# Kernel tuning notes

Hardware: AMD Instinct MI355X
Metric: run time of the kernel (lower is better)

Reference implementation:

```python
import jax, jax.numpy as jnp
import numpy as np

D = 256; H = 8; L = 4; P = 4; DFF = 1024
B = 4; NQ = 900
SHAPES = np.array([[100, 160], [50, 80], [25, 40], [13, 20]], dtype=np.int64)
NV = int((SHAPES[:, 0] * SHAPES[:, 1]).sum())


def setup_inputs():
    key = jax.random.key(0)
    ks = jax.random.split(key, 16)
    def w(k, shape):
        return jax.random.normal(k, shape, jnp.float32) * 0.02
    return {
        "tgt": jax.random.normal(ks[0], (B, NQ, D), jnp.float32),
        "tgt_query_pos": jax.random.normal(ks[1], (B, NQ, D), jnp.float32),
        "tgt_reference_points": jax.random.uniform(ks[2], (B, NQ, L, 2), dtype=jnp.float32),
        "memory": jax.random.normal(ks[3], (B, NV, D), jnp.float32),
        "value_proj_w": w(ks[4], (D, D)), "value_proj_b": jnp.zeros((D,), jnp.float32),
        "samp_off_w": w(ks[5], (H * L * P * 2, D)), "samp_off_b": jnp.zeros((H * L * P * 2,), jnp.float32),
        "attn_w_w": w(ks[6], (H * L * P, D)), "attn_w_b": jnp.zeros((H * L * P,), jnp.float32),
        "ca_out_w": w(ks[7], (D, D)), "ca_out_b": jnp.zeros((D,), jnp.float32),
        "ln1_g": jnp.ones((D,), jnp.float32), "ln1_b": jnp.zeros((D,), jnp.float32),
        "in_proj_w": w(ks[8], (3 * D, D)), "in_proj_b": jnp.zeros((3 * D,), jnp.float32),
        "sa_out_w": w(ks[9], (D, D)), "sa_out_b": jnp.zeros((D,), jnp.float32),
        "ln2_g": jnp.ones((D,), jnp.float32), "ln2_b": jnp.zeros((D,), jnp.float32),
        "ffn1_w": w(ks[10], (DFF, D)), "ffn1_b": jnp.zeros((DFF,), jnp.float32),
        "ffn2_w": w(ks[11], (D, DFF)), "ffn2_b": jnp.zeros((D,), jnp.float32),
        "ln3_g": jnp.ones((D,), jnp.float32), "ln3_b": jnp.zeros((D,), jnp.float32),
        "spatial_shapes": jnp.asarray(SHAPES),
    }


def layer_norm(x, g, b, eps=1e-5):
    m = x.mean(-1, keepdims=True)
    v = ((x - m) ** 2).mean(-1, keepdims=True)
    return (x - m) / jnp.sqrt(v + eps) * g + b


def ms_deform_attn(query, refp, value, shapes, Wv, bv, Wo, bo, Wa, ba, Wout, bout):
    # query [B,Nq,D], refp [B,Nq,L,2] in [0,1], value [B,NV,D]; shapes: np [L,2] (H,W)
    Bq, Nq, Dm = query.shape
    dh = Dm // H
    v = (value @ Wv.T + bv).reshape(Bq, -1, H, dh)
    off = (query @ Wo.T + bo).reshape(Bq, Nq, H, L, P, 2)
    aw = jax.nn.softmax((query @ Wa.T + ba).reshape(Bq, Nq, H, L * P), axis=-1)
    aw = aw.reshape(Bq, Nq, H, L, P)
    norm = jnp.asarray(np.stack([shapes[:, 1], shapes[:, 0]], -1), jnp.float32)  # [L,2] = (W,H)
    loc = refp[:, :, None, :, None, :] + off / norm[None, None, None, :, None, :]  # [B,Nq,H,L,P,2]
    starts = np.concatenate([[0], np.cumsum(shapes[:, 0] * shapes[:, 1])])
    acc = jnp.zeros((Bq, Nq, H, dh), query.dtype)
    for l in range(L):
        Hl, Wl = int(shapes[l, 0]), int(shapes[l, 1])
        vf = v[:, int(starts[l]):int(starts[l]) + Hl * Wl]                 # [B,HW,H,dh]
        v2 = vf.transpose(0, 2, 1, 3).reshape(Bq * H, Hl * Wl, dh)
        # grid_sample align_corners=False: pixel = loc*size - 0.5
        xl = loc[:, :, :, l, :, 0] * Wl - 0.5                              # [B,Nq,H,P]
        yl = loc[:, :, :, l, :, 1] * Hl - 0.5
        x0 = jnp.floor(xl); y0 = jnp.floor(yl)
        wx = xl - x0; wy = yl - y0
        x0i = x0.astype(jnp.int32); y0i = y0.astype(jnp.int32)
        def corner(xi, yi, wgt):
            valid = (xi >= 0) & (xi < Wl) & (yi >= 0) & (yi < Hl)
            idx = jnp.clip(yi, 0, Hl - 1) * Wl + jnp.clip(xi, 0, Wl - 1)   # [B,Nq,H,P]
            idx2 = idx.transpose(0, 2, 1, 3).reshape(Bq * H, Nq * P)
            g = jnp.take_along_axis(v2, idx2[..., None], axis=1)           # [B*H,Nq*P,dh]
            g = g.reshape(Bq, H, Nq, P, dh).transpose(0, 2, 1, 3, 4)
            return g * (wgt * valid).astype(query.dtype)[..., None]
        s = (corner(x0i, y0i, (1 - wx) * (1 - wy))
             + corner(x0i + 1, y0i, wx * (1 - wy))
             + corner(x0i, y0i + 1, (1 - wx) * wy)
             + corner(x0i + 1, y0i + 1, wx * wy))                          # [B,Nq,H,P,dh]
        acc = acc + jnp.einsum('bqhpd,bqhp->bqhd', s, aw[:, :, :, l])
    return acc.reshape(Bq, Nq, Dm) @ Wout.T + bout


def mha(q, k, v, Win, bin_, Wout, bout):
    Dm = q.shape[-1]; dh = Dm // H
    def proj(x, W, b):
        return (x @ W.T + b).reshape(x.shape[0], x.shape[1], H, dh)
    qh = proj(q, Win[:Dm], bin_[:Dm])
    kh = proj(k, Win[Dm:2 * Dm], bin_[Dm:2 * Dm])
    vh = proj(v, Win[2 * Dm:], bin_[2 * Dm:])
    att = jax.nn.softmax(jnp.einsum('bqhd,bkhd->bhqk', qh, kh) / np.sqrt(dh).astype(np.float32), axis=-1)
    o = jnp.einsum('bhqk,bkhd->bqhd', att, vh).reshape(q.shape[0], q.shape[1], Dm)
    return o @ Wout.T + bout


def _forward(tgt, tgt_query_pos, tgt_reference_points, memory,
             value_proj_w, value_proj_b, samp_off_w, samp_off_b, attn_w_w, attn_w_b,
             ca_out_w, ca_out_b, ln1_g, ln1_b, in_proj_w, in_proj_b, sa_out_w, sa_out_b,
             ln2_g, ln2_b, ffn1_w, ffn1_b, ffn2_w, ffn2_b, ln3_g, ln3_b, shapes):
    # cross (deformable) attention
    q = tgt + tgt_query_pos
    tgt2 = ms_deform_attn(q, tgt_reference_points, memory, shapes,
                          value_proj_w, value_proj_b, samp_off_w, samp_off_b,
                          attn_w_w, attn_w_b, ca_out_w, ca_out_b)
    x = layer_norm(tgt + tgt2, ln1_g, ln1_b)
    # self attention (q=k=x+pos, v=x)
    qk = x + tgt_query_pos
    x = layer_norm(x + mha(qk, qk, x, in_proj_w, in_proj_b, sa_out_w, sa_out_b), ln2_g, ln2_b)
    # FFN
    ff = jax.nn.relu(x @ ffn1_w.T + ffn1_b) @ ffn2_w.T + ffn2_b
    return layer_norm(x + ff, ln3_g, ln3_b)


def reference(tgt, tgt_query_pos, tgt_reference_points, memory,
              value_proj_w, value_proj_b, samp_off_w, samp_off_b, attn_w_w, attn_w_b,
              ca_out_w, ca_out_b, ln1_g, ln1_b, in_proj_w, in_proj_b, sa_out_w, sa_out_b,
              ln2_g, ln2_b, ffn1_w, ffn1_b, ffn2_w, ffn2_b, ln3_g, ln3_b, spatial_shapes):
    shapes = np.asarray(spatial_shapes)
    return _forward(tgt, tgt_query_pos, tgt_reference_points, memory,
                    value_proj_w, value_proj_b, samp_off_w, samp_off_b, attn_w_w, attn_w_b,
                    ca_out_w, ca_out_b, ln1_g, ln1_b, in_proj_w, in_proj_b, sa_out_w, sa_out_b,
                    ln2_g, ln2_b, ffn1_w, ffn1_b, ffn2_w, ffn2_b, ln3_g, ln3_b, shapes)
```

## Files before the change

kernel.cpp:

```cpp
#include <hip/hip_runtime.h>

constexpr int D_   = 256;
constexpr int H_   = 8;
constexpr int DH   = 32;
constexpr int L_   = 4;
constexpr int P_   = 4;
constexpr int DFF_ = 1024;
constexpr int B_   = 4;
constexpr int NQ_  = 900;
constexpr int NV_  = 21260;
constexpr int MQ   = B_ * NQ_;
constexpr int MV   = B_ * NV_;

typedef __attribute__((ext_vector_type(8))) short short8;
typedef __attribute__((ext_vector_type(4))) float f32x4;

static __device__ __forceinline__ unsigned short f2bf(float x) {
  union { float f; unsigned int u; } v;
  v.f = x;
  const unsigned int r = v.u + 0x7fffu + ((v.u >> 16) & 1u);
  return (unsigned short)(r >> 16);
}
static __device__ __forceinline__ float bf2f(unsigned short u) {
  union { unsigned int i; float f; } x;
  x.i = ((unsigned int)u) << 16;
  return x.f;
}

struct CvtArgs {
  const float* src[9];
  unsigned short* dst[9];
  int n[9];
  float scl[9];
};

__global__ __launch_bounds__(256) void cvtw(CvtArgs a) {
  const int seg = blockIdx.y;
  const int n = a.n[seg];
  const float s = a.scl[seg];
  const float* __restrict__ sp = a.src[seg];
  unsigned short* __restrict__ d = a.dst[seg];
  for (int i = (blockIdx.x * 256 + threadIdx.x) * 4; i < n;
       i += gridDim.x * 256 * 4) {
    const float4 v = *reinterpret_cast<const float4*>(&sp[i]);
    d[i + 0] = f2bf(v.x * s); d[i + 1] = f2bf(v.y * s);
    d[i + 2] = f2bf(v.z * s); d[i + 3] = f2bf(v.w * s);
  }
}

__global__ void biasprep(const float* __restrict__ bin,
                         const float* __restrict__ bo,
                         const float* __restrict__ ba,
                         float* __restrict__ bqkv, float* __restrict__ bfu) {
  const int i = threadIdx.x;
  if (i < 768) bqkv[i] = (i < 256) ? bin[i] * 0.17677669529663687f : bin[i];
  if (i < 384) bfu[i] = (i < 256) ? bo[i] : ba[i - 256];
}

template <bool ABF, bool ADD2, bool RELU, bool OUTBF>
__global__ __launch_bounds__(256) void gemm_db(
    const void* __restrict__ Ap, const float* __restrict__ A2,
    const unsigned short* __restrict__ Wbf, const float* __restrict__ bias,
    void* __restrict__ Cp, int M, int N, int K) {
  constexpr int LDR = 40;
  __shared__ unsigned short As[2][128][LDR];
  __shared__ unsigned short Bs[2][128][LDR];

  const float* Af = (const float*)Ap;
  const unsigned short* Ab = (const unsigned short*)Ap;
  float* Cf = (float*)Cp;
  unsigned short* Cb = (unsigned short*)Cp;

  const int t    = threadIdx.x;
  const int wave = t >> 6;
  const int l    = t & 63;
  const int n0   = blockIdx.x * 128;
  const int m0   = blockIdx.y * 128;
  const int wm   = (wave >> 1) * 64;
  const int wn   = (wave & 1) * 64;
  const int srow = t >> 1;
  const int sseg = (t & 1) * 16;
  const int lr   = l & 15;
  const int lk   = (l >> 4) * 8;

  const int am = m0 + srow;
  const bool aok = am < M;
  const size_t arow = (size_t)am * K;
  const size_t brow = (size_t)(n0 + srow) * K;

  f32x4 acc[4][4];
#pragma unroll
  for (int i = 0; i < 4; ++i)
#pragma unroll
    for (int j = 0; j < 4; ++j) acc[i][j] = (f32x4)0.f;

  short8 ar0, ar1, br0, br1;

  auto LOAD = [&](int k0) {
    if constexpr (ABF) {
      if (aok) {
        ar0 = *reinterpret_cast<const short8*>(&Ab[arow + k0 + sseg]);
        ar1 = *reinterpret_cast<const short8*>(&Ab[arow + k0 + sseg + 8]);
      } else {
        ar0 = (short8)(short)0; ar1 = (short8)(short)0;
      }
    } else {
      if (aok) {
        float f[16];
#pragma unroll
        for (int j = 0; j < 4; ++j) {
          const float4 av =
              *reinterpret_cast<const float4*>(&Af[arow + k0 + sseg + 4 * j]);
          f[4 * j + 0] = av.x; f[4 * j + 1] = av.y;
          f[4 * j + 2] = av.z; f[4 * j + 3] = av.w;
        }
        if constexpr (ADD2) {
#pragma unroll
          for (int j = 0; j < 4; ++j) {
            const float4 av =
                *reinterpret_cast<const float4*>(&A2[arow + k0 + sseg + 4 * j]);
            f[4 * j + 0] += av.x; f[4 * j + 1] += av.y;
            f[4 * j + 2] += av.z; f[4 * j + 3] += av.w;
          }
        }
        alignas(16) unsigned short u[16];
#pragma unroll
        for (int j = 0; j < 16; ++j) u[j] = f2bf(f[j]);
        ar0 = *reinterpret_cast<short8*>(&u[0]);
        ar1 = *reinterpret_cast<short8*>(&u[8]);
      } else {
        ar0 = (short8)(short)0; ar1 = (short8)(short)0;
      }
    }
    br0 = *reinterpret_cast<const short8*>(&Wbf[brow + k0 + sseg]);
    br1 = *reinterpret_cast<const short8*>(&Wbf[brow + k0 + sseg + 8]);
  };

  const int nt = K >> 5;
  LOAD(0);
  for (int tt = 0; tt < nt; ++tt) {
    const int cur = tt & 1;
    *reinterpret_cast<short8*>(&As[cur][srow][sseg])     = ar0;
    *reinterpret_cast<short8*>(&As[cur][srow][sseg + 8]) = ar1;
    *reinterpret_cast<short8*>(&Bs[cur][srow][sseg])     = br0;
    *reinterpret_cast<short8*>(&Bs[cur][srow][sseg + 8]) = br1;
    if (tt + 1 < nt) LOAD((tt + 1) << 5);
    __syncthreads();

    short8 af[4], bfr[4];
#pragma unroll
    for (int fi = 0; fi < 4; ++fi)
      af[fi] = *reinterpret_cast<const short8*>(&As[cur][wm + fi * 16 + lr][lk]);
#pragma unroll
    for (int fj = 0; fj < 4; ++fj)
      bfr[fj] = *reinterpret_cast<const short8*>(&Bs[cur][wn + fj * 16 + lr][lk]);

#pragma unroll
    for (int fi = 0; fi < 4; ++fi)
#pragma unroll
      for (int fj = 0; fj < 4; ++fj)
        acc[fi][fj] = __builtin_amdgcn_mfma_f32_16x16x32_bf16(
            af[fi], bfr[fj], acc[fi][fj], 0, 0, 0);
  }

  const int orow = (l >> 4) * 4;
#pragma unroll
  for (int fi = 0; fi < 4; ++fi) {
#pragma unroll
    for (int fj = 0; fj < 4; ++fj) {
      const int n = n0 + wn + fj * 16 + lr;
      const float bn = bias[n];
#pragma unroll
      for (int i = 0; i < 4; ++i) {
        const int m = m0 + wm + fi * 16 + orow + i;
        if (m < M) {
          float vv = acc[fi][fj][i] + bn;
          if (RELU) vv = fmaxf(vv, 0.f);
          if (OUTBF)
            Cb[(size_t)m * N + n] = f2bf(vv);
          else
            Cf[(size_t)m * N + n] = vv;
        }
      }
    }
  }
}

template <int K, bool ABF, bool ADD2, bool RELU, bool OUTBF>
__global__ __launch_bounds__(256) void gemm_p2(
    const void* __restrict__ Ap, const float* __restrict__ A2,
    const unsigned short* __restrict__ Wbf, const float* __restrict__ bias,
    void* __restrict__ Cp, int M, int N) {
  constexpr int LDR = 40;
  constexpr int NT = K / 32;
  __shared__ unsigned short As[2][128][LDR];
  __shared__ unsigned short Bs[2][128][LDR];

  const float* Af = (const float*)Ap;
  const unsigned short* Ab = (const unsigned short*)Ap;
  float* Cf = (float*)Cp;
  unsigned short* Cb = (unsigned short*)Cp;

  const int t    = threadIdx.x;
  const int wave = t >> 6;
  const int l    = t & 63;
  const int n0   = blockIdx.x * 128;
  const int m0   = blockIdx.y * 128;
  const int wm   = (wave >> 1) * 64;
  const int wn   = (wave & 1) * 64;
  const int srow = t >> 1;
  const int sseg = (t & 1) * 16;
  const int lr   = l & 15;
  const int lk   = (l >> 4) * 8;

  const int am = m0 + srow;
  const bool aok = am < M;
  const size_t arow = (size_t)am * K;
  const size_t brow = (size_t)(n0 + srow) * K;

  f32x4 acc[4][4];
#pragma unroll
  for (int i = 0; i < 4; ++i)
#pragma unroll
    for (int j = 0; j < 4; ++j) acc[i][j] = (f32x4)0.f;

  float  frA[16], frB[16];
  short8 abA0, abA1, abB0, abB1;
  short8 brA0, brA1, brB0, brB1;

#define LOAD_SLOT(SUF, k0)                                                     \
  do {                                                                         \
    if constexpr (ABF) {                                                       \
      if (aok) {                                                               \
        ab##SUF##0 = *reinterpret_cast<const short8*>(&Ab[arow + (k0) + sseg]);\
        ab##SUF##1 = *reinterpret_cast<const short8*>(&Ab[arow + (k0) + sseg + 8]);\
      } else {                                                                 \
        ab##SUF##0 = (short8)(short)0; ab##SUF##1 = (short8)(short)0;          \
      }                                                                        \
    } else {                                                                   \
      if (aok) {                                                               \
        _Pragma("unroll")                                                      \
        for (int j = 0; j < 4; ++j) {                                          \
          const float4 av =                                                    \
              *reinterpret_cast<const float4*>(&Af[arow + (k0) + sseg + 4 * j]);\
          fr##SUF[4 * j + 0] = av.x; fr##SUF[4 * j + 1] = av.y;                \
          fr##SUF[4 * j + 2] = av.z; fr##SUF[4 * j + 3] = av.w;                \
        }                                                                      \
        if constexpr (ADD2) {                                                  \
          _Pragma("unroll")                                                    \
          for (int j = 0; j < 4; ++j) {                                        \
            const float4 av =                                                  \
                *reinterpret_cast<const float4*>(&A2[arow + (k0) + sseg + 4 * j]);\
            fr##SUF[4 * j + 0] += av.x; fr##SUF[4 * j + 1] += av.y;            \
            fr##SUF[4 * j + 2] += av.z; fr##SUF[4 * j + 3] += av.w;            \
          }                                                                    \
        }                                                                      \
      } else {                                                                 \
        _Pragma("unroll")                                                      \
        for (int j = 0; j < 16; ++j) fr##SUF[j] = 0.f;                         \
      }                                                                        \
    }                                                                          \
    br##SUF##0 = *reinterpret_cast<const short8*>(&Wbf[brow + (k0) + sseg]);   \
    br##SUF##1 = *reinterpret_cast<const short8*>(&Wbf[brow + (k0) + sseg + 8]);\
  } while (0)

#define WRITE_SLOT(SUF, BUF)                                                   \
  do {                                                                         \
    if constexpr (ABF) {                                                       \
      *reinterpret_cast<short8*>(&As[BUF][srow][sseg])     = ab##SUF##0;       \
      *reinterpret_cast<short8*>(&As[BUF][srow][sseg + 8]) = ab##SUF##1;       \
    } else {                                                                   \
      alignas(16) unsigned short u[16];                                        \
      _Pragma("unroll")                                                        \
      for (int j = 0; j < 16; ++j) u[j] = f2bf(fr##SUF[j]);                    \
      *reinterpret_cast<short8*>(&As[BUF][srow][sseg]) =                       \
          *reinterpret_cast<short8*>(&u[0]);                                   \
      *reinterpret_cast<short8*>(&As[BUF][srow][sseg + 8]) =                   \
          *reinterpret_cast<short8*>(&u[8]);                                   \
    }                                                                          \
    *reinterpret_cast<short8*>(&Bs[BUF][srow][sseg])     = br##SUF##0;         \
    *reinterpret_cast<short8*>(&Bs[BUF][srow][sseg + 8]) = br##SUF##1;         \
  } while (0)

#define MFMA_STEP(BUF)                                                         \
  do {                                                                         \
    short8 af0 = *reinterpret_cast<const short8*>(&As[BUF][wm +  0 + lr][lk]); \
    short8 af1 = *reinterpret_cast<const short8*>(&As[BUF][wm + 16 + lr][lk]); \
    short8 af2 = *reinterpret_cast<const short8*>(&As[BUF][wm + 32 + lr][lk]); \
    short8 af3 = *reinterpret_cast<const short8*>(&As[BUF][wm + 48 + lr][lk]); \
    short8 bf0 = *reinterpret_cast<const short8*>(&Bs[BUF][wn +  0 + lr][lk]); \
    short8 bf1 = *reinterpret_cast<const short8*>(&Bs[BUF][wn + 16 + lr][lk]); \
    short8 bf2 = *reinterpret_cast<const short8*>(&Bs[BUF][wn + 32 + lr][lk]); \
    short8 bf3 = *reinterpret_cast<const short8*>(&Bs[BUF][wn + 48 + lr][lk]); \
    acc[0][0] = __builtin_amdgcn_mfma_f32_16x16x32_bf16(af0, bf0, acc[0][0], 0, 0, 0); \
    acc[0][1] = __builtin_amdgcn_mfma_f32_16x16x32_bf16(af0, bf1, acc[0][1], 0, 0, 0); \
    acc[0][2] = __builtin_amdgcn_mfma_f32_16x16x32_bf16(af0, bf2, acc[0][2], 0, 0, 0); \
    acc[0][3] = __builtin_amdgcn_mfma_f32_16x16x32_bf16(af0, bf3, acc[0][3], 0, 0, 0); \
    acc[1][0] = __builtin_amdgcn_mfma_f32_16x16x32_bf16(af1, bf0, acc[1][0], 0, 0, 0); \
    acc[1][1] = __builtin_amdgcn_mfma_f32_16x16x32_bf16(af1, bf1, acc[1][1], 0, 0, 0); \
    acc[1][2] = __builtin_amdgcn_mfma_f32_16x16x32_bf16(af1, bf2, acc[1][2], 0, 0, 0); \
    acc[1][3] = __builtin_amdgcn_mfma_f32_16x16x32_bf16(af1, bf3, acc[1][3], 0, 0, 0); \
    acc[2][0] = __builtin_amdgcn_mfma_f32_16x16x32_bf16(af2, bf0, acc[2][0], 0, 0, 0); \
    acc[2][1] = __builtin_amdgcn_mfma_f32_16x16x32_bf16(af2, bf1, acc[2][1], 0, 0, 0); \
    acc[2][2] = __builtin_amdgcn_mfma_f32_16x16x32_bf16(af2, bf2, acc[2][2], 0, 0, 0); \
    acc[2][3] = __builtin_amdgcn_mfma_f32_16x16x32_bf16(af2, bf3, acc[2][3], 0, 0, 0); \
    acc[3][0] = __builtin_amdgcn_mfma_f32_16x16x32_bf16(af3, bf0, acc[3][0], 0, 0, 0); \
    acc[3][1] = __builtin_amdgcn_mfma_f32_16x16x32_bf16(af3, bf1, acc[3][1], 0, 0, 0); \
    acc[3][2] = __builtin_amdgcn_mfma_f32_16x16x32_bf16(af3, bf2, acc[3][2], 0, 0, 0); \
    acc[3][3] = __builtin_amdgcn_mfma_f32_16x16x32_bf16(af3, bf3, acc[3][3], 0, 0, 0); \
  } while (0)

  LOAD_SLOT(A, 0);
  LOAD_SLOT(B, 32);
#pragma unroll
  for (int tt = 0; tt < NT; tt += 2) {
    WRITE_SLOT(A, 0);
    if (tt + 2 < NT) LOAD_SLOT(A, (tt + 2) * 32);
    __syncthreads();
    MFMA_STEP(0);

    WRITE_SLOT(B, 1);
    if (tt + 3 < NT) LOAD_SLOT(B, (tt + 3) * 32);
    __syncthreads();
    MFMA_STEP(1);
  }
#undef LOAD_SLOT
#undef WRITE_SLOT
#undef MFMA_STEP

  const int orow = (l >> 4) * 4;
#pragma unroll
  for (int fi = 0; fi < 4; ++fi) {
#pragma unroll
    for (int fj = 0; fj < 4; ++fj) {
      const int n = n0 + wn + fj * 16 + lr;
      const float bn = bias[n];
#pragma unroll
      for (int i = 0; i < 4; ++i) {
        const int m = m0 + wm + fi * 16 + orow + i;
        if (m < M) {
          float vv = acc[fi][fj][i] + bn;
          if (RELU) vv = fmaxf(vv, 0.f);
          if (OUTBF)
            Cb[(size_t)m * N + n] = f2bf(vv);
          else
            Cf[(size_t)m * N + n] = vv;
        }
      }
    }
  }
}

template <bool ABF, bool ADD2, bool RELU, bool OUTBF>
__global__ __launch_bounds__(256) void gemm_bres(
    const void* __restrict__ Ap, const float* __restrict__ A2,
    const unsigned short* __restrict__ Wbf, const float* __restrict__ bias,
    void* __restrict__ Cp, int M, int N, int add_nlim) {
  __shared__ unsigned short Bs[32768];
  __shared__ unsigned short As[2][64][40];

  const float* Af = (const float*)Ap;
  const unsigned short* Ab = (const unsigned short*)Ap;
  float* Cf = (float*)Cp;
  unsigned short* Cb = (unsigned short*)Cp;

  const int t    = threadIdx.x;
  const int wave = t >> 6;
  const int l    = t & 63;
  const int n0   = blockIdx.x * 128;
  const int m0   = blockIdx.y * 64;
  const int wm   = (wave >> 1) * 32;
  const int wcg  = (wave & 1) * 4;
  const int lr   = l & 15;
  const int lk8  = (l >> 4) * 8;
  const bool doadd = ADD2 && (n0 < add_nlim);

#pragma unroll
  for (int i = 0; i < 16; ++i) {
    const int e  = i * 256 + t;
    const int el = e & 63;
    const int cg = (e >> 6) & 7;
    const int st = e >> 9;
    const int row = n0 + cg * 16 + (el & 15);
    const int col = st * 32 + ((el >> 4) * 8);
    *reinterpret_cast<short8*>(&Bs[e * 8]) =
        *reinterpret_cast<const short8*>(&Wbf[(size_t)row * 256 + col]);
  }

  const int arow = t >> 2;
  const int acol = (t & 3) * 8;
  const int am   = m0 + arow;
  const bool aok = am < M;
  const size_t abase = (size_t)am * 256 + acol;

  float  fr[3][8];
  short8 br_[3];

  auto ALOAD = [&](int slot, int tt) {
    const int k0 = tt * 32;
    if constexpr (ABF) {
      br_[slot] = aok ? *reinterpret_cast<const short8*>(&Ab[abase + k0])
                      : (short8)(short)0;
    } else {
      if (aok) {
        const float4 a0 = *reinterpret_cast<const float4*>(&Af[abase + k0]);
        const float4 a1 = *reinterpret_cast<const float4*>(&Af[abase + k0 + 4]);
        fr[slot][0] = a0.x; fr[slot][1] = a0.y;
        fr[slot][2] = a0.z; fr[slot][3] = a0.w;
        fr[slot][4] = a1.x; fr[slot][5] = a1.y;
        fr[slot][6] = a1.z; fr[slot][7] = a1.w;
        if constexpr (ADD2) {
          if (doadd) {
            const float4 b0 = *reinterpret_cast<const float4*>(&A2[abase + k0]);
            const float4 b1 = *reinterpret_cast<const float4*>(&A2[abase + k0 + 4]);
            fr[slot][0] += b0.x; fr[slot][1] += b0.y;
            fr[slot][2] += b0.z; fr[slot][3] += b0.w;
            fr[slot][4] += b1.x; fr[slot][5] += b1.y;
            fr[slot][6] += b1.z; fr[slot][7] += b1.w;
          }
        }
      } else {
#pragma unroll
        for (int j = 0; j < 8; ++j) fr[slot][j] = 0.f;
      }
    }
  };
  auto AWRITE = [&](int slot, int tt) {
    if constexpr (ABF) {
      *reinterpret_cast<short8*>(&As[tt & 1][arow][acol]) = br_[slot];
    } else {
      alignas(16) unsigned short u[8];
#pragma unroll
      for (int j = 0; j < 8; ++j) u[j] = f2bf(fr[slot][j]);
      *reinterpret_cast<short8*>(&As[tt & 1][arow][acol]) =
          *reinterpret_cast<short8*>(&u[0]);
    }
  };

  f32x4 acc[2][4];
#pragma unroll
  for (int fi = 0; fi < 2; ++fi)
#pragma unroll
    for (int fj = 0; fj < 4; ++fj) acc[fi][fj] = (f32x4)0.f;

  ALOAD(0, 0); ALOAD(1, 1); ALOAD(2, 2);

#pragma unroll
  for (int tt = 0; tt < 8; ++tt) {
    AWRITE(tt % 3, tt);
    if (tt + 3 < 8) ALOAD(tt % 3, tt + 3);
    __syncthreads();

    short8 afr[2];
#pragma unroll
    for (int fi = 0; fi < 2; ++fi)
      afr[fi] = *reinterpret_cast<const short8*>(&As[tt & 1][wm + fi * 16 + lr][lk8]);

#pragma unroll
    for (int fj = 0; fj < 4; ++fj) {
      const short8 bfr = *reinterpret_cast<const short8*>(
          &Bs[(((tt * 8) + wcg + fj) * 64 + l) * 8]);
      acc[0][fj] = __builtin_amdgcn_mfma_f32_16x16x32_bf16(afr[0], bfr, acc[0][fj], 0, 0, 0);
      acc[1][fj] = __builtin_amdgcn_mfma_f32_16x16x32_bf16(afr[1], bfr, acc[1][fj], 0, 0, 0);
    }
  }

  const int or4 = (l >> 4) * 4;
#pragma unroll
  for (int fi = 0; fi < 2; ++fi) {
#pragma unroll
    for (int fj = 0; fj < 4; ++fj) {
      const int n = n0 + (wave & 1) * 64 + fj * 16 + lr;
      const float bn = bias[n];
#pragma unroll
      for (int i = 0; i < 4; ++i) {
        const int m = m0 + wm + fi * 16 + or4 + i;
        if (m < M) {
          float vv = acc[fi][fj][i] + bn;
          if (RELU) vv = fmaxf(vv, 0.f);
          if (OUTBF)
            Cb[(size_t)m * N + n] = f2bf(vv);
          else
            Cf[(size_t)m * N + n] = vv;
        }
      }
    }
  }
}

__global__ __launch_bounds__(256) void deform(const float* __restrict__ refp,
                                              const float* __restrict__ offlog,
                                              const unsigned short* __restrict__ v,
                                              float* __restrict__ acc) {
  __shared__ float aw[2][128];
  const int t  = threadIdx.x;
  const int tq = t >> 7;
  const int tt = t & 127;
  const int bq = blockIdx.x * 2 + tq;
  const int b  = bq / NQ_;
  const int h  = tt >> 4;
  const int dd = tt & 15;

  aw[tq][tt] = offlog[(size_t)bq * 384 + 256 + tt];
  __syncthreads();
  if (t < 16) {
    const int q = t >> 3, hh = t & 7;
    float* a = &aw[q][hh * 16];
    float mx = -1e30f;
#pragma unroll
    for (int i = 0; i < 16; ++i) mx = fmaxf(mx, a[i]);
    float e[16], s = 0.f;
#pragma unroll
    for (int i = 0; i < 16; ++i) { e[i] = expf(a[i] - mx); s += e[i]; }
    const float inv = 1.f / s;
#pragma unroll
    for (int i = 0; i < 16; ++i) a[i] = e[i] * inv;
  }
  __syncthreads();

  constexpr int ST[4] = {0, 16000, 20000, 21000};
  constexpr int HL[4] = {100, 50, 25, 13};
  constexpr int WL[4] = {160, 80, 40, 20};

  float a0 = 0.f, a1 = 0.f;
#pragma unroll
  for (int l = 0; l < L_; ++l) {
    const float rx = refp[(bq * L_ + l) * 2 + 0];
    const float ry = refp[(bq * L_ + l) * 2 + 1];
    const float Wf = (float)WL[l], Hf = (float)HL[l];
    const int   Wi = WL[l], Hi = HL[l];
    const size_t vbase = (size_t)(b * NV_ + ST[l]) * D_ + h * DH + dd * 2;
#pragma unroll
    for (int p = 0; p < P_; ++p) {
      const float ox = offlog[(size_t)bq * 384 + h * 32 + l * 8 + p * 2 + 0];
      const float oy = offlog[(size_t)bq * 384 + h * 32 + l * 8 + p * 2 + 1];
      const float locx = rx + ox / Wf;
      const float locy = ry + oy / Hf;
      const float xl = locx * Wf - 0.5f;
      const float yl = locy * Hf - 0.5f;
      const float x0 = floorf(xl), y0 = floorf(yl);
      const float wx = xl - x0, wy = yl - y0;
      const int x0i = (int)x0, y0i = (int)y0;
      const float w = aw[tq][h * 16 + l * 4 + p];

      float s0 = 0.f, s1 = 0.f;
#pragma unroll
      for (int c = 0; c < 4; ++c) {
        const int xi = x0i + (c & 1);
        const int yi = y0i + (c >> 1);
        const float cw = ((c & 1) ? wx : 1.f - wx) * ((c >> 1) ? wy : 1.f - wy);
        const bool valid = (xi >= 0) && (xi < Wi) && (yi >= 0) && (yi < Hi);
        const int xc = min(max(xi, 0), Wi - 1);
        const int yc = min(max(yi, 0), Hi - 1);
        const unsigned int g2 = *reinterpret_cast<const unsigned int*>(
            &v[vbase + (size_t)(yc * Wi + xc) * D_]);
        const float g0 = bf2f((unsigned short)(g2 & 0xffffu));
        const float g1 = bf2f((unsigned short)(g2 >> 16));
        s0 += valid ? g0 * cw : 0.f;
        s1 += valid ? g1 * cw : 0.f;
      }
      a0 += w * s0;
      a1 += w * s1;
    }
  }
  acc[(size_t)bq * D_ + h * DH + dd * 2 + 0] = a0;
  acc[(size_t)bq * D_ + h * DH + dd * 2 + 1] = a1;
}

constexpr int TQM  = 64;
constexpr int NQTM = (NQ_ + TQM - 1) / TQM;

__global__ __launch_bounds__(256) void mha_mfma(
    const unsigned short* __restrict__ qkvh,
    unsigned short* __restrict__ o) {
  __shared__ unsigned short Qs[64][40];
  __shared__ unsigned short Ks[64][40];
  __shared__ unsigned short Vts[32][72];
  __shared__ unsigned short Ps[64][72];

  const int bx = blockIdx.x;
  const int qt = bx % NQTM;
  const int h  = (bx / NQTM) % H_;
  const int b  = bx / (NQTM * H_);
  const int t  = threadIdx.x;
  const int wave = t >> 6;
  const int l    = t & 63;
  const int q0   = qt * TQM;
  const int wrow = wave * 16;
  const int lr   = l & 15;
  const int lkb  = (l >> 4) * 8;

  {
    const int r = t >> 2, cb = (t & 3) * 8;
    short8 u;
    if (q0 + r < NQ_)
      u = *reinterpret_cast<const short8*>(
          &qkvh[(size_t)(b * NQ_ + q0 + r) * 768 + h * DH + cb]);
    else
      u = (short8)(short)0;
    *reinterpret_cast<short8*>(&Qs[r][cb]) = u;
  }
  __syncthreads();

  const short8 qa = *reinterpret_cast<const short8*>(&Qs[wrow + lr][lkb]);

  f32x4 oacc[2];
  oacc[0] = (f32x4)0.f; oacc[1] = (f32x4)0.f;
  float m_[4] = {-1e30f, -1e30f, -1e30f, -1e30f};
  float l_[4] = {0.f, 0.f, 0.f, 0.f};

  for (int kt = 0; kt < NQTM; ++kt) {
    const int k0 = kt * 64;
    const int nk = min(64, NQ_ - k0);
    __syncthreads();

    {
      const int r = t >> 2, cb = (t & 3) * 8;
      short8 u;
      if (r < nk)
        u = *reinterpret_cast<const short8*>(
            &qkvh[(size_t)(b * NQ_ + k0 + r) * 768 + 256 + h * DH + cb]);
      else
        u = (short8)(short)0;
      *reinterpret_cast<short8*>(&Ks[r][cb]) = u;
    }
    {
      const int k = t & 63, db = (t >> 6) * 8;
      short8 u;
      if (k < nk)
        u = *reinterpret_cast<const short8*>(
            &qkvh[(size_t)(b * NQ_ + k0 + k) * 768 + 512 + h * DH + db]);
      else
        u = (short8)(short)0;
#pragma unroll
      for (int j = 0; j < 8; ++j) Vts[db + j][k] = (unsigned short)u[j];
    }
    __syncthreads();

    f32x4 sacc[4];
#pragma unroll
    for (int fj = 0; fj < 4; ++fj)
      sacc[fj] = __builtin_amdgcn_mfma_f32_16x16x32_bf16(
          qa, *reinterpret_cast<const short8*>(&Ks[16 * fj + lr][lkb]),
          (f32x4)0.f, 0, 0, 0);

    bool cv[4];
#pragma unroll
    for (int fj = 0; fj < 4; ++fj) cv[fj] = (16 * fj + lr) < nk;

    float p0[4], p1[4], p2[4], p3[4], sc_[4];
#pragma unroll
    for (int i = 0; i < 4; ++i) {
      float tm = -1e30f;
      if (cv[0]) tm = fmaxf(tm, sacc[0][i]);
      if (cv[1]) tm = fmaxf(tm, sacc[1][i]);
      if (cv[2]) tm = fmaxf(tm, sacc[2][i]);
      if (cv[3]) tm = fmaxf(tm, sacc[3][i]);
      tm = fmaxf(tm, __shfl_xor(tm, 1));
      tm = fmaxf(tm, __shfl_xor(tm, 2));
      tm = fmaxf(tm, __shfl_xor(tm, 4));
      tm = fmaxf(tm, __shfl_xor(tm, 8));
      const float mn = fmaxf(m_[i], tm);
      sc_[i] = __expf(m_[i] - mn);
      m_[i] = mn;
      const float e0 = cv[0] ? __expf(sacc[0][i] - mn) : 0.f;
      const float e1 = cv[1] ? __expf(sacc[1][i] - mn) : 0.f;
      const float e2 = cv[2] ? __expf(sacc[2][i] - mn) : 0.f;
      const float e3 = cv[3] ? __expf(sacc[3][i] - mn) : 0.f;
      p0[i] = e0; p1[i] = e1; p2[i] = e2; p3[i] = e3;
      float rs = e0 + e1 + e2 + e3;
      rs += __shfl_xor(rs, 1);
      rs += __shfl_xor(rs, 2);
      rs += __shfl_xor(rs, 4);
      rs += __shfl_xor(rs, 8);
      l_[i] = l_[i] * sc_[i] + rs;
    }

#pragma unroll
    for (int i = 0; i < 4; ++i) {
      const int pr = wrow + (l >> 4) * 4 + i;
      Ps[pr][0  + lr] = f2bf(p0[i]);
      Ps[pr][16 + lr] = f2bf(p1[i]);
      Ps[pr][32 + lr] = f2bf(p2[i]);
      Ps[pr][48 + lr] = f2bf(p3[i]);
    }
    __syncthreads();

    const short8 pa0 = *reinterpret_cast<const short8*>(&Ps[wrow + lr][lkb]);
    const short8 pa1 = *reinterpret_cast<const short8*>(&Ps[wrow + lr][lkb + 32]);
#pragma unroll
    for (int nt = 0; nt < 2; ++nt) {
      f32x4 c = oacc[nt];
#pragma unroll
      for (int i = 0; i < 4; ++i) c[i] *= sc_[i];
      c = __builtin_amdgcn_mfma_f32_16x16x32_bf16(
          pa0, *reinterpret_cast<const short8*>(&Vts[16 * nt + lr][lkb]), c, 0, 0, 0);
      c = __builtin_amdgcn_mfma_f32_16x16x32_bf16(
          pa1, *reinterpret_cast<const short8*>(&Vts[16 * nt + lr][lkb + 32]), c, 0, 0, 0);
      oacc[nt] = c;
    }
  }

#pragma unroll
  for (int i = 0; i < 4; ++i) {
    const int r = (l >> 4) * 4 + i;
    const int q = q0 + wrow + r;
    if (q < NQ_) {
      const float inv = 1.f / l_[i];
      o[(size_t)(b * NQ_ + q) * D_ + h * DH + 0  + lr] = f2bf(oacc[0][i] * inv);
      o[(size_t)(b * NQ_ + q) * D_ + h * DH + 16 + lr] = f2bf(oacc[1][i] * inv);
    }
  }
}

__global__ __launch_bounds__(256) void ln(const float* __restrict__ res,
                                          const float* __restrict__ add,
                                          const float* __restrict__ g,
                                          const float* __restrict__ bt,
                                          float* __restrict__ out) {
  __shared__ float red[256];
  const int r = blockIdx.x, t = threadIdx.x;
  const float x = res[r * D_ + t] + add[r * D_ + t];
  red[t] = x;
  __syncthreads();
  for (int s = 128; s > 0; s >>= 1) {
    if (t < s) red[t] += red[t + s];
    __syncthreads();
  }
  const float mean = red[0] * (1.f / D_);
  __syncthreads();
  const float dx = x - mean;
  red[t] = dx * dx;
  __syncthreads();
  for (int s = 128; s > 0; s >>= 1) {
    if (t < s) red[t] += red[t + s];
    __syncthreads();
  }
  const float var = red[0] * (1.f / D_);
  out[r * D_ + t] = dx * rsqrtf(var + 1e-5f) * g[t] + bt[t];
}

extern "C" void kernel_launch(void* const* d_in, const int* in_sizes, int n_in,
                              void* d_out, int out_size, void* d_ws,
                              size_t ws_size, hipStream_t stream) {
  const float* tgt   = (const float*)d_in[0];
  const float* pos   = (const float*)d_in[1];
  const float* refp  = (const float*)d_in[2];
  const float* mem   = (const float*)d_in[3];
  const float* Wv    = (const float*)d_in[4];
  const float* bv    = (const float*)d_in[5];
  const float* Wo    = (const float*)d_in[6];
  const float* bo    = (const float*)d_in[7];
  const float* Wa    = (const float*)d_in[8];
  const float* ba    = (const float*)d_in[9];
  const float* Wca   = (const float*)d_in[10];
  const float* bca   = (const float*)d_in[11];
  const float* g1    = (const float*)d_in[12];
  const float* b1    = (const float*)d_in[13];
  const float* Win   = (const float*)d_in[14];
  const float* bin   = (const float*)d_in[15];
  const float* Wsa   = (const float*)d_in[16];
  const float* bsa   = (const float*)d_in[17];
  const float* g2    = (const float*)d_in[18];
  const float* b2    = (const float*)d_in[19];
  const float* W1    = (const float*)d_in[20];
  const float* bb1   = (const float*)d_in[21];
  const float* W2    = (const float*)d_in[22];
  const float* bb2   = (const float*)d_in[23];
  const float* g3    = (const float*)d_in[24];
  const float* b3    = (const float*)d_in[25];

  char* cur = (char*)d_ws;
  auto alloc = [&](size_t bytes) {
    char* p = cur;
    cur += (bytes + 255) & ~(size_t)255;
    return (void*)p;
  };
  unsigned short* v_bf    = (unsigned short*)alloc((size_t)MV * 256 * 2);
  float*          offlog  = (float*)alloc((size_t)MQ * 384 * 4);
  float*          accb    = (float*)alloc((size_t)MQ * 256 * 4);
  float*          tmp     = (float*)alloc((size_t)MQ * 256 * 4);
  float*          x1      = (float*)alloc((size_t)MQ * 256 * 4);
  float*          x2      = (float*)alloc((size_t)MQ * 256 * 4);
  unsigned short* qkvh_bf = (unsigned short*)alloc((size_t)MQ * 768 * 2);
  unsigned short* obuf_bf = (unsigned short*)alloc((size_t)MQ * 256 * 2);
  unsigned short* h1_bf   = (unsigned short*)alloc((size_t)MQ * 1024 * 2);
  unsigned short* Wv_bf   = (unsigned short*)alloc(65536 * 2);
  unsigned short* Wfu_bf  = (unsigned short*)alloc(98304 * 2);
  unsigned short* Wca_bf  = (unsigned short*)alloc(65536 * 2);
  unsigned short* Win_bf  = (unsigned short*)alloc(196608 * 2);
  unsigned short* Wsa_bf  = (unsigned short*)alloc(65536 * 2);
  unsigned short* W1_bf   = (unsigned short*)alloc(262144 * 2);
  unsigned short* W2_bf   = (unsigned short*)alloc(262144 * 2);
  float*          biasqkv = (float*)alloc(768 * 4);
  float*          bfused  = (float*)alloc(384 * 4);

  const float qscale = 0.17677669529663687f;

  CvtArgs ca;
  ca.src[0] = Wv;            ca.dst[0] = Wv_bf;          ca.n[0] = 65536;  ca.scl[0] = 1.f;
  ca.src[1] = Wo;            ca.dst[1] = Wfu_bf;         ca.n[1] = 65536;  ca.scl[1] = 1.f;
  ca.src[2] = Wa;            ca.dst[2] = Wfu_bf + 65536; ca.n[2] = 32768;  ca.scl[2] = 1.f;
  ca.src[3] = Wca;           ca.dst[3] = Wca_bf;         ca.n[3] = 65536;  ca.scl[3] = 1.f;
  ca.src[4] = Win;           ca.dst[4] = Win_bf;         ca.n[4] = 65536;  ca.scl[4] = qscale;
  ca.src[5] = Win + 65536;   ca.dst[5] = Win_bf + 65536; ca.n[5] = 131072; ca.scl[5] = 1.f;
  ca.src[6] = Wsa;           ca.dst[6] = Wsa_bf;         ca.n[6] = 65536;  ca.scl[6] = 1.f;
  ca.src[7] = W1;            ca.dst[7] = W1_bf;          ca.n[7] = 262144; ca.scl[7] = 1.f;
  ca.src[8] = W2;            ca.dst[8] = W2_bf;          ca.n[8] = 262144; ca.scl[8] = 1.f;
  cvtw<<<dim3(64, 9), 256, 0, stream>>>(ca);
  biasprep<<<1, 768, 0, stream>>>(bin, bo, ba, biasqkv, bfused);

  const int mqb64  = (MQ + 63) / 64;
  const int mvb128 = (MV + 127) / 128;

  gemm_db<false, false, false, true><<<dim3(2, mvb128), 256, 0, stream>>>(
      mem, nullptr, Wv_bf, bv, v_bf, MV, 256, 256);
  gemm_bres<false, true, false, false><<<dim3(3, mqb64), 256, 0, stream>>>(
      tgt, pos, Wfu_bf, bfused, offlog, MQ, 384, 384);
  deform<<<MQ / 2, 256, 0, stream>>>(refp, offlog, v_bf, accb);
  gemm_bres<false, false, false, false><<<dim3(2, mqb64), 256, 0, stream>>>(
      accb, nullptr, Wca_bf, bca, tmp, MQ, 256, 0);
  ln<<<MQ, 256, 0, stream>>>(tgt, tmp, g1, b1, x1);
  gemm_bres<false, true, false, true><<<dim3(6, mqb64), 256, 0, stream>>>(
      x1, pos, Win_bf, biasqkv, qkvh_bf, MQ, 768, 512);
  mha_mfma<<<B_ * H_ * NQTM, 256, 0, stream>>>(qkvh_bf, obuf_bf);
  gemm_bres<true, false, false, false><<<dim3(2, mqb64), 256, 0, stream>>>(
      obuf_bf, nullptr, Wsa_bf, bsa, tmp, MQ, 256, 0);
  ln<<<MQ, 256, 0, stream>>>(x1, tmp, g2, b2, x2);
  gemm_bres<false, false, true, true><<<dim3(8, mqb64), 256, 0, stream>>>(
      x2, nullptr, W1_bf, bb1, h1_bf, MQ, 1024, 0);
  gemm_p2<1024, true, false, false, false><<<dim3(2, (MQ + 127) / 128), 256, 0, stream>>>(
      h1_bf, nullptr, W2_bf, bb2, tmp, MQ, 256);
  ln<<<MQ, 256, 0, stream>>>(x2, tmp, g3, b3, (float*)d_out);
}
```

Before: 214.3 us.

## Store deform output in bf16, prefetch K/V in MHA, use wave-per-row LayerNorm

The deformable-attention kernel now writes its accumulator as packed bf16, so the following output-projection GEMM reads bf16 input instead of fp32. In the MHA kernel, K/V tiles for the next iteration are loaded into registers while the current tile is being computed, and one __syncthreads is removed. The LayerNorm kernel is replaced by one that gives each row to a single wave, using float4 loads and shuffle reductions instead of a shared-memory tree reduction. The bf16 accumulator lowers precision. Removing the barrier before the Ps reads relies on each wave reading only its own rows of Ps.

```diff
diff --git a/kernel.cpp b/kernel.cpp
--- a/kernel.cpp
+++ b/kernel.cpp
@@ -491,7 +491,7 @@
 __global__ __launch_bounds__(256) void deform(const float* __restrict__ refp,
                                               const float* __restrict__ offlog,
                                               const unsigned short* __restrict__ v,
-                                              float* __restrict__ acc) {
+                                              unsigned int* __restrict__ accb2) {
   __shared__ float aw[2][128];
   const int t  = threadIdx.x;
   const int tq = t >> 7;
@@ -563,8 +563,9 @@
       a1 += w * s1;
     }
   }
-  acc[(size_t)bq * D_ + h * DH + dd * 2 + 0] = a0;
-  acc[(size_t)bq * D_ + h * DH + dd * 2 + 1] = a1;
+  const unsigned int packed =
+      (unsigned int)f2bf(a0) | ((unsigned int)f2bf(a1) << 16);
+  accb2[((size_t)bq * D_ + h * DH + dd * 2) >> 1] = packed;
 }
 
 constexpr int TQM  = 64;
@@ -590,16 +591,31 @@
   const int lr   = l & 15;
   const int lkb  = (l >> 4) * 8;
 
+  const int kr = t >> 2, kcb = (t & 3) * 8;
+  const int vk = t & 63, vdb = (t >> 6) * 8;
+
+  short8 ku, vu;
+  auto LOADKV = [&](int kt) {
+    const int k0 = kt * 64;
+    const int nk = min(64, NQ_ - k0);
+    ku = (kr < nk) ? *reinterpret_cast<const short8*>(
+                         &qkvh[(size_t)(b * NQ_ + k0 + kr) * 768 + 256 + h * DH + kcb])
+                   : (short8)(short)0;
+    vu = (vk < nk) ? *reinterpret_cast<const short8*>(
+                         &qkvh[(size_t)(b * NQ_ + k0 + vk) * 768 + 512 + h * DH + vdb])
+                   : (short8)(short)0;
+  };
+
   {
-    const int r = t >> 2, cb = (t & 3) * 8;
     short8 u;
-    if (q0 + r < NQ_)
+    if (q0 + kr < NQ_)
       u = *reinterpret_cast<const short8*>(
-          &qkvh[(size_t)(b * NQ_ + q0 + r) * 768 + h * DH + cb]);
+          &qkvh[(size_t)(b * NQ_ + q0 + kr) * 768 + h * DH + kcb]);
     else
       u = (short8)(short)0;
-    *reinterpret_cast<short8*>(&Qs[r][cb]) = u;
-  }
+    *reinterpret_cast<short8*>(&Qs[kr][kcb]) = u;
+  }
+  LOADKV(0);
   __syncthreads();
 
   const short8 qa = *reinterpret_cast<const short8*>(&Qs[wrow + lr][lkb]);
@@ -614,27 +630,11 @@
     const int nk = min(64, NQ_ - k0);
     __syncthreads();
 
-    {
-      const int r = t >> 2, cb = (t & 3) * 8;
-      short8 u;
-      if (r < nk)
-        u = *reinterpret_cast<const short8*>(
-            &qkvh[(size_t)(b * NQ_ + k0 + r) * 768 + 256 + h * DH + cb]);
-      else
-        u = (short8)(short)0;
-      *reinterpret_cast<short8*>(&Ks[r][cb]) = u;
-    }
-    {
-      const int k = t & 63, db = (t >> 6) * 8;
-      short8 u;
-      if (k < nk)
-        u = *reinterpret_cast<const short8*>(
-            &qkvh[(size_t)(b * NQ_ + k0 + k) * 768 + 512 + h * DH + db]);
-      else
-        u = (short8)(short)0;
-#pragma unroll
-      for (int j = 0; j < 8; ++j) Vts[db + j][k] = (unsigned short)u[j];
-    }
+    *reinterpret_cast<short8*>(&Ks[kr][kcb]) = ku;
+#pragma unroll
+    for (int j = 0; j < 8; ++j) Vts[vdb + j][vk] = (unsigned short)vu[j];
+
+    if (kt + 1 < NQTM) LOADKV(kt + 1);
     __syncthreads();
 
     f32x4 sacc[4];
@@ -684,7 +684,6 @@
       Ps[pr][32 + lr] = f2bf(p2[i]);
       Ps[pr][48 + lr] = f2bf(p3[i]);
     }
-    __syncthreads();
 
     const short8 pa0 = *reinterpret_cast<const short8*>(&Ps[wrow + lr][lkb]);
     const short8 pa1 = *reinterpret_cast<const short8*>(&Ps[wrow + lr][lkb + 32]);
@@ -713,31 +712,39 @@
   }
 }
 
-__global__ __launch_bounds__(256) void ln(const float* __restrict__ res,
-                                          const float* __restrict__ add,
-                                          const float* __restrict__ g,
-                                          const float* __restrict__ bt,
-                                          float* __restrict__ out) {
-  __shared__ float red[256];
-  const int r = blockIdx.x, t = threadIdx.x;
-  const float x = res[r * D_ + t] + add[r * D_ + t];
-  red[t] = x;
-  __syncthreads();
-  for (int s = 128; s > 0; s >>= 1) {
-    if (t < s) red[t] += red[t + s];
-    __syncthreads();
-  }
-  const float mean = red[0] * (1.f / D_);
-  __syncthreads();
-  const float dx = x - mean;
-  red[t] = dx * dx;
-  __syncthreads();
-  for (int s = 128; s > 0; s >>= 1) {
-    if (t < s) red[t] += red[t + s];
-    __syncthreads();
-  }
-  const float var = red[0] * (1.f / D_);
-  out[r * D_ + t] = dx * rsqrtf(var + 1e-5f) * g[t] + bt[t];
+__global__ __launch_bounds__(256) void ln4(const float* __restrict__ res,
+                                           const float* __restrict__ add,
+                                           const float* __restrict__ g,
+                                           const float* __restrict__ bt,
+                                           float* __restrict__ out) {
+  const int wave = threadIdx.x >> 6, lane = threadIdx.x & 63;
+  const int r = blockIdx.x * 4 + wave;
+  const size_t base = (size_t)r * D_ + lane * 4;
+  const float4 a = *reinterpret_cast<const float4*>(&res[base]);
+  const float4 bv = *reinterpret_cast<const float4*>(&add[base]);
+  float4 x;
+  x.x = a.x + bv.x; x.y = a.y + bv.y; x.z = a.z + bv.z; x.w = a.w + bv.w;
+
+  float s = x.x + x.y + x.z + x.w;
+#pragma unroll
+  for (int off = 1; off < 64; off <<= 1) s += __shfl_xor(s, off);
+  const float mean = s * (1.f / D_);
+
+  const float dx0 = x.x - mean, dx1 = x.y - mean, dx2 = x.z - mean,
+              dx3 = x.w - mean;
+  float v = dx0 * dx0 + dx1 * dx1 + dx2 * dx2 + dx3 * dx3;
+#pragma unroll
+  for (int off = 1; off < 64; off <<= 1) v += __shfl_xor(v, off);
+  const float rstd = rsqrtf(v * (1.f / D_) + 1e-5f);
+
+  const float4 gg = *reinterpret_cast<const float4*>(&g[lane * 4]);
+  const float4 bb = *reinterpret_cast<const float4*>(&bt[lane * 4]);
+  float4 o;
+  o.x = dx0 * rstd * gg.x + bb.x;
+  o.y = dx1 * rstd * gg.y + bb.y;
+  o.z = dx2 * rstd * gg.z + bb.z;
+  o.w = dx3 * rstd * gg.w + bb.w;
+  *reinterpret_cast<float4*>(&out[base]) = o;
 }
 
 extern "C" void kernel_launch(void* const* d_in, const int* in_sizes, int n_in,
@@ -778,7 +785,7 @@
   };
   unsigned short* v_bf    = (unsigned short*)alloc((size_t)MV * 256 * 2);
   float*          offlog  = (float*)alloc((size_t)MQ * 384 * 4);
-  float*          accb    = (float*)alloc((size_t)MQ * 256 * 4);
+  unsigned short* accb_bf = (unsigned short*)alloc((size_t)MQ * 256 * 2);
   float*          tmp     = (float*)alloc((size_t)MQ * 256 * 4);
   float*          x1      = (float*)alloc((size_t)MQ * 256 * 4);
   float*          x2      = (float*)alloc((size_t)MQ * 256 * 4);
@@ -817,19 +824,20 @@
       mem, nullptr, Wv_bf, bv, v_bf, MV, 256, 256);
   gemm_bres<false, true, false, false><<<dim3(3, mqb64), 256, 0, stream>>>(
       tgt, pos, Wfu_bf, bfused, offlog, MQ, 384, 384);
-  deform<<<MQ / 2, 256, 0, stream>>>(refp, offlog, v_bf, accb);
-  gemm_bres<false, false, false, false><<<dim3(2, mqb64), 256, 0, stream>>>(
-      accb, nullptr, Wca_bf, bca, tmp, MQ, 256, 0);
-  ln<<<MQ, 256, 0, stream>>>(tgt, tmp, g1, b1, x1);
+  deform<<<MQ / 2, 256, 0, stream>>>(refp, offlog, v_bf,
+                                     (unsigned int*)accb_bf);
+  gemm_bres<true, false, false, false><<<dim3(2, mqb64), 256, 0, stream>>>(
+      accb_bf, nullptr, Wca_bf, bca, tmp, MQ, 256, 0);
+  ln4<<<MQ / 4, 256, 0, stream>>>(tgt, tmp, g1, b1, x1);
   gemm_bres<false, true, false, true><<<dim3(6, mqb64), 256, 0, stream>>>(
       x1, pos, Win_bf, biasqkv, qkvh_bf, MQ, 768, 512);
   mha_mfma<<<B_ * H_ * NQTM, 256, 0, stream>>>(qkvh_bf, obuf_bf);
   gemm_bres<true, false, false, false><<<dim3(2, mqb64), 256, 0, stream>>>(
       obuf_bf, nullptr, Wsa_bf, bsa, tmp, MQ, 256, 0);
-  ln<<<MQ, 256, 0, stream>>>(x1, tmp, g2, b2, x2);
+  ln4<<<MQ / 4, 256, 0, stream>>>(x1, tmp, g2, b2, x2);
   gemm_bres<false, false, true, true><<<dim3(8, mqb64), 256, 0, stream>>>(
       x2, nullptr, W1_bf, bb1, h1_bf, MQ, 1024, 0);
   gemm_p2<1024, true, false, false, false><<<dim3(2, (MQ + 127) / 128), 256, 0, stream>>>(
       h1_bf, nullptr, W2_bf, bb2, tmp, MQ, 256);
-  ln<<<MQ, 256, 0, stream>>>(x2, tmp, g3, b3, (float*)d_out);
-}
+  ln4<<<MQ / 4, 256, 0, stream>>>(x2, tmp, g3, b3, (float*)d_out);
+}
```

Result: faster. 201.1 us (-6.1%).
